# Optimization experiments

Hardware: AMD Instinct MI355X
Metric: run time of the kernel (lower is better)

## Reference

```python
import jax, jax.numpy as jnp
import numpy as np

N_FEATURES = 170
D_MODEL = 64
N_HEADS = 4
ALPHA = 0.1
LN_EPS = 1e-5
LEAKY_SLOPE = 0.01  # torch F.leaky_relu default
N = 3 * N_FEATURES  # 510
B = 32


def setup_inputs() -> dict:
    key = jax.random.key(0)
    ks = jax.random.split(key, 10)
    D, H = D_MODEL, N_HEADS
    s = 1.0 / np.sqrt(D)
    return {
        "x": jax.random.normal(ks[0], (B, N, D), dtype=jnp.float32),
        "causal_graph": jax.random.uniform(ks[1], (N, N), dtype=jnp.float32),
        # nn.Linear(d_model, d_model*n_heads, bias=False): stored here as (D, H*D) for x @ W
        "W": jax.random.uniform(ks[2], (D, H * D), jnp.float32, -s, s),
        "attention_w": jax.random.normal(ks[3], (H, 2 * D), dtype=jnp.float32),
        # Conv2d(2, n_heads, 3, padding=1): OIHW kernel
        "conv_w": jax.random.uniform(ks[4], (H, 2, 3, 3), jnp.float32, -1/np.sqrt(18), 1/np.sqrt(18)),
        "conv_b": jax.random.uniform(ks[5], (H,), jnp.float32, -1/np.sqrt(18), 1/np.sqrt(18)),
        # nn.Linear(d_model, 2*d_model): stored as (D, 2D)
        "fcg_w": jax.random.uniform(ks[6], (D, 2 * D), jnp.float32, -s, s),
        "fcg_b": jax.random.uniform(ks[7], (2 * D,), jnp.float32, -s, s),
        "ln_g": jnp.ones((D,), jnp.float32),
        "ln_b": jnp.zeros((D,), jnp.float32),
    }


def reference(x, causal_graph, W, attention_w, conv_w, conv_b, fcg_w, fcg_b, ln_g, ln_b):
    Bz, Nn, D = x.shape
    H = N_HEADS
    # shared projection: (B, N, H, D)
    xt = (x @ W).reshape(Bz, Nn, H, D)
    # GAT-style additive scores: concat-dot decomposed into two dot products
    w1, w2 = attention_w[:, :D], attention_w[:, D:]  # each (H, D)
    s_i = jnp.einsum('bnhd,hd->bhn', xt, w1)  # source term
    s_j = jnp.einsum('bnhd,hd->bhn', xt, w2)  # target term
    e = s_i[:, :, :, None] + s_j[:, :, None, :]  # (B, H, N, N)
    A_eva = jnp.where(e >= 0, e, LEAKY_SLOPE * e)  # leaky_relu
    # fuse mean attention with causal graph via 3x3 conv
    A_mean = A_eva.mean(axis=1)  # (B, N, N)
    causal = jnp.broadcast_to(causal_graph[None], (Bz, Nn, Nn))
    stacked = jnp.stack([A_mean, causal], axis=1)  # (B, 2, N, N)
    A_st = jax.lax.conv_general_dilated(
        stacked, conv_w, window_strides=(1, 1), padding=((1, 1), (1, 1)),
        dimension_numbers=('NCHW', 'OIHW', 'NCHW'))
    A_st = A_st + conv_b[None, :, None, None]  # (B, H, N, N)
    A = jax.nn.softmax(ALPHA * A_eva + (1.0 - ALPHA) * A_st, axis=-1)
    # multi-head aggregation then head-mean
    out = jnp.einsum('bhnm,bmhd->bnhd', A, xt).mean(axis=2)  # (B, N, D)
    # GLU
    g = out @ fcg_w + fcg_b  # (B, N, 2D)
    a, b = g[..., :D], g[..., D:]
    glu = a * jax.nn.sigmoid(b)
    # residual + layernorm
    y = glu + x
    mu = y.mean(axis=-1, keepdims=True)
    var = ((y - mu) ** 2).mean(axis=-1, keepdims=True)
    y = (y - mu) * jax.lax.rsqrt(var + LN_EPS) * ln_g + ln_b
    return y, A
```

## Files before the change

### kernel.cpp

```cpp
#include <hip/hip_runtime.h>

#define Bz 32
#define Nn 510
#define Dd 64
#define Hh 4
#define HD_ 256
#define Kpad 512
#define ALPHA_ 0.1f
#define LNEPS 1e-5f
#define SLOPE 0.01f
#define NEG_INF -3.0e38f

typedef __attribute__((ext_vector_type(8))) short short8;
typedef __attribute__((ext_vector_type(4))) float floatx4;

__device__ inline float wredsum(float v) {
  #pragma unroll
  for (int off = 32; off; off >>= 1) v += __shfl_xor(v, off, 64);
  return v;
}
__device__ inline float wredmax(float v) {
  #pragma unroll
  for (int off = 32; off; off >>= 1) v = fmaxf(v, __shfl_xor(v, off, 64));
  return v;
}
__device__ inline unsigned short f2bf(float f) {
  unsigned int u = __float_as_uint(f);
  unsigned int r = (u + 0x7fffu + ((u >> 16) & 1u)) >> 16;
  return (unsigned short)r;
}

__global__ __launch_bounds__(256) void k1_xt(const float* __restrict__ x,
                                             const float* __restrict__ W,
                                             const float* __restrict__ attw,
                                             unsigned short* __restrict__ xtT,
                                             float* __restrict__ si,
                                             float* __restrict__ sj) {
  __shared__ float Wl[64][132];
  __shared__ float xr[32][68];
  const int t = threadIdx.x;
  const int rt = blockIdx.x;
  const int b = blockIdx.y;
  const int ch = blockIdx.z;
  #pragma unroll
  for (int k = 0; k < 8; k++) {
    int f = t + k * 256;
    int kr = f >> 5;
    int c = (f & 31) * 4;
    float4 v = *(const float4*)&W[kr * HD_ + ch * 128 + c];
    *(float4*)&Wl[kr][c] = v;
  }
  #pragma unroll
  for (int k = 0; k < 2; k++) {
    int f = t + k * 256;
    int r = f >> 4;
    int c = (f & 15) * 4;
    int row = rt * 32 + r;
    float4 v = make_float4(0.f, 0.f, 0.f, 0.f);
    if (row < Nn) v = *(const float4*)&x[(b * Nn + row) * Dd + c];
    *(float4*)&xr[r][c] = v;
  }
  __syncthreads();
  const int tr = t >> 5, tc = t & 31;
  const int rb = tr * 4, c0 = tc * 4;
  float acc[4][4] = {};
  #pragma unroll
  for (int k4 = 0; k4 < 16; k4++) {
    float4 xv[4];
    #pragma unroll
    for (int r = 0; r < 4; r++) xv[r] = *(float4*)&xr[rb + r][k4 * 4];
    #pragma unroll
    for (int kk = 0; kk < 4; kk++) {
      float4 wv = *(float4*)&Wl[k4 * 4 + kk][c0];
      #pragma unroll
      for (int r = 0; r < 4; r++) {
        float xs = (&xv[r].x)[kk];
        acc[r][0] = fmaf(xs, wv.x, acc[r][0]);
        acc[r][1] = fmaf(xs, wv.y, acc[r][1]);
        acc[r][2] = fmaf(xs, wv.z, acc[r][2]);
        acc[r][3] = fmaf(xs, wv.w, acc[r][3]);
      }
    }
  }
  const int colbase = ch * 128 + c0;
  const int h = colbase >> 6;
  const int dd = colbase & 63;
  const int m0r = rt * 32 + rb;
  #pragma unroll
  for (int cc = 0; cc < 4; cc++) {
    unsigned short* p = &xtT[((size_t)(b * 4 + h) * 64 + (dd + cc)) * Kpad + m0r];
    if (m0r + 3 < Nn) {
      ushort4 u;
      u.x = f2bf(acc[0][cc]); u.y = f2bf(acc[1][cc]);
      u.z = f2bf(acc[2][cc]); u.w = f2bf(acc[3][cc]);
      *(ushort4*)p = u;
    } else {
      #pragma unroll
      for (int r = 0; r < 4; r++) if (m0r + r < Nn) p[r] = f2bf(acc[r][cc]);
    }
  }
  float w1v[4], w2v[4];
  #pragma unroll
  for (int cc = 0; cc < 4; cc++) {
    w1v[cc] = attw[h * 128 + dd + cc];
    w2v[cc] = attw[h * 128 + 64 + dd + cc];
  }
  #pragma unroll
  for (int r = 0; r < 4; r++) {
    float p1 = acc[r][0] * w1v[0] + acc[r][1] * w1v[1] +
               acc[r][2] * w1v[2] + acc[r][3] * w1v[3];
    float p2 = acc[r][0] * w2v[0] + acc[r][1] * w2v[1] +
               acc[r][2] * w2v[2] + acc[r][3] * w2v[3];
    #pragma unroll
    for (int off = 1; off <= 8; off <<= 1) {
      p1 += __shfl_xor(p1, off, 64);
      p2 += __shfl_xor(p2, off, 64);
    }
    if ((tc & 15) == 0) {
      int row = m0r + r;
      if (row < Nn) {
        si[(b * 4 + h) * Nn + row] = p1;
        sj[(b * 4 + h) * Nn + row] = p2;
      }
    }
  }
}

__global__ __launch_bounds__(256) void k2_attn(const float* __restrict__ si,
                                               const float* __restrict__ sj,
                                               const float* __restrict__ causal,
                                               const float* __restrict__ convw,
                                               const float* __restrict__ convb,
                                               float* __restrict__ A) {
  __shared__ float amr[3][520];
  __shared__ float c3[3][520];
  const int t = threadIdx.x;
  const int i = blockIdx.x;
  const int b = blockIdx.y;
  for (int e = t; e < 3 * 520; e += 256) {
    int row = e / 520;
    int jj = e - row * 520;
    int iq = i + row - 1;
    int j = jj - 1;
    float am = 0.f, cz = 0.f;
    if (jj < 512 && iq >= 0 && iq < Nn && j >= 0 && j < Nn) {
      float s = 0.f;
      #pragma unroll
      for (int hh = 0; hh < 4; hh++) {
        float e2 = si[(b * 4 + hh) * Nn + iq] + sj[(b * 4 + hh) * Nn + j];
        s += (e2 >= 0.f) ? e2 : SLOPE * e2;
      }
      am = 0.25f * s;
      cz = causal[iq * Nn + j];
    }
    amr[row][jj] = am;
    c3[row][jj] = cz;
  }
  __syncthreads();
  const int h = t >> 6;
  const int lane = t & 63;
  const int j0 = lane * 8;
  const int bh = b * 4 + h;
  const float sih = si[bh * Nn + i];
  float cw[18];
  #pragma unroll
  for (int q = 0; q < 18; q++) cw[q] = convw[h * 18 + q];
  float conv[8];
  const float cb = convb[h];
  #pragma unroll
  for (int e = 0; e < 8; e++) conv[e] = cb;
  #pragma unroll
  for (int di = 0; di < 3; di++) {
    float ta[12], tcc[12];
    *(float4*)&ta[0] = *(float4*)&amr[di][j0];
    *(float4*)&ta[4] = *(float4*)&amr[di][j0 + 4];
    *(float4*)&ta[8] = *(float4*)&amr[di][j0 + 8];
    *(float4*)&tcc[0] = *(float4*)&c3[di][j0];
    *(float4*)&tcc[4] = *(float4*)&c3[di][j0 + 4];
    *(float4*)&tcc[8] = *(float4*)&c3[di][j0 + 8];
    float w0 = cw[di * 3], w1 = cw[di * 3 + 1], w2 = cw[di * 3 + 2];
    float u0 = cw[9 + di * 3], u1 = cw[9 + di * 3 + 1], u2 = cw[9 + di * 3 + 2];
    #pragma unroll
    for (int e = 0; e < 8; e++) {
      float cv = conv[e];
      cv = fmaf(w0, ta[e], cv);
      cv = fmaf(w1, ta[e + 1], cv);
      cv = fmaf(w2, ta[e + 2], cv);
      cv = fmaf(u0, tcc[e], cv);
      cv = fmaf(u1, tcc[e + 1], cv);
      cv = fmaf(u2, tcc[e + 2], cv);
      conv[e] = cv;
    }
  }
  float sjv[8];
  {
    const float* sp = &sj[bh * Nn + j0];
    *(float2*)&sjv[0] = *(const float2*)&sp[0];
    *(float2*)&sjv[2] = *(const float2*)&sp[2];
    *(float2*)&sjv[4] = *(const float2*)&sp[4];
    *(float2*)&sjv[6] = *(const float2*)&sp[6];
  }
  float v[8];
  float mx = NEG_INF;
  #pragma unroll
  for (int e = 0; e < 8; e++) {
    float ee = sih + sjv[e];
    float l = (ee >= 0.f) ? ee : SLOPE * ee;
    float val = ALPHA_ * l + (1.0f - ALPHA_) * conv[e];
    v[e] = (j0 + e < Nn) ? val : NEG_INF;
    mx = fmaxf(mx, v[e]);
  }
  mx = wredmax(mx);
  float p[8], s = 0.f;
  #pragma unroll
  for (int e = 0; e < 8; e++) {
    p[e] = __expf(v[e] - mx);
    s += p[e];
  }
  s = wredsum(s);
  const float inv = 1.f / s;
  float* Ar = &A[((size_t)bh * Nn + i) * Nn];
  #pragma unroll
  for (int pr = 0; pr < 4; pr++) {
    if (j0 + 2 * pr + 1 < Nn) {
      float2 w2v = make_float2(p[2 * pr] * inv, p[2 * pr + 1] * inv);
      *(float2*)&Ar[j0 + 2 * pr] = w2v;
    }
  }
}

__global__ __launch_bounds__(256) void k3_out(const float* __restrict__ A,
                                              const unsigned short* __restrict__ xtT,
                                              const float* __restrict__ x,
                                              const float* __restrict__ fcgw,
                                              const float* __restrict__ fcgb,
                                              const float* __restrict__ lng,
                                              const float* __restrict__ lnb,
                                              float* __restrict__ y) {
  __shared__ unsigned short Asub[32 * 72];
  __shared__ unsigned short Xsub[64 * 72];
  __shared__ float ol[32][64];
  __shared__ float gl[2][128];
  const int t = threadIdx.x;
  const int n0 = blockIdx.x * 32;
  const int b = blockIdx.y;
  const int w = t >> 6, lane = t & 63;
  const int quad = lane >> 4, l16 = lane & 15;
  const int wr = (w & 1) * 16;
  const int wc = (w >> 1) * 32;
  const int ar = t >> 3;
  const int amc = (t & 7) * 8;
  const int xd = t >> 2;
  const int xmc = (t & 3) * 16;
  floatx4 acc0 = {0.f, 0.f, 0.f, 0.f};
  floatx4 acc1 = {0.f, 0.f, 0.f, 0.f};
  for (int h = 0; h < 4; h++) {
    const float* Ab = &A[((size_t)(b * 4 + h) * Nn + n0) * Nn];
    const unsigned short* Xb = &xtT[(size_t)(b * 4 + h) * 64 * Kpad];
    for (int kt = 0; kt < 8; kt++) {
      const int m0 = kt * 64;
      __syncthreads();
      {
        int n = n0 + ar;
        int m = m0 + amc;
        float av[8] = {0.f, 0.f, 0.f, 0.f, 0.f, 0.f, 0.f, 0.f};
        if (n < Nn) {
          const float* src = &Ab[(size_t)ar * Nn + m];
          if (m + 7 < Nn) {
            #pragma unroll
            for (int q = 0; q < 4; q++) *(float2*)&av[2 * q] = *(const float2*)&src[2 * q];
          } else {
            int lim = Nn - m;
            #pragma unroll
            for (int q = 0; q < 8; q++) if (q < lim) av[q] = src[q];
          }
        }
        short8 as;
        #pragma unroll
        for (int q = 0; q < 8; q++) as[q] = (short)f2bf(av[q]);
        *(short8*)&Asub[ar * 72 + amc] = as;
        const unsigned short* xs = &Xb[(size_t)xd * Kpad + m0 + xmc];
        short8 x0 = *(const short8*)&xs[0];
        short8 x1 = *(const short8*)&xs[8];
        *(short8*)&Xsub[xd * 72 + xmc] = x0;
        *(short8*)&Xsub[xd * 72 + xmc + 8] = x1;
      }
      __syncthreads();
      #pragma unroll
      for (int ks = 0; ks < 2; ks++) {
        short8 af = *(short8*)&Asub[(wr + l16) * 72 + ks * 32 + quad * 8];
        short8 b0 = *(short8*)&Xsub[(wc + l16) * 72 + ks * 32 + quad * 8];
        short8 b1 = *(short8*)&Xsub[(wc + 16 + l16) * 72 + ks * 32 + quad * 8];
        acc0 = __builtin_amdgcn_mfma_f32_16x16x32_bf16(af, b0, acc0, 0, 0, 0);
        acc1 = __builtin_amdgcn_mfma_f32_16x16x32_bf16(af, b1, acc1, 0, 0, 0);
      }
    }
  }
  __syncthreads();
  #pragma unroll
  for (int reg = 0; reg < 4; reg++) {
    ol[wr + quad * 4 + reg][wc + l16] = 0.25f * acc0[reg];
    ol[wr + quad * 4 + reg][wc + 16 + l16] = 0.25f * acc1[reg];
  }
  __syncthreads();
  const int kk = t & 127;
  const int rg = t >> 7;
  for (int it = 0; it < 16; it++) {
    const int r = it * 2 + rg;
    const int row = n0 + r;
    float g = fcgb[kk];
    #pragma unroll
    for (int d = 0; d < 64; d++) g = fmaf(ol[r][d], fcgw[d * 128 + kk], g);
    gl[rg][kk] = g;
    __syncthreads();
    if (kk < 64 && row < Nn) {
      float a = gl[rg][kk];
      float bb = gl[rg][kk + 64];
      float glu = a / (1.f + __expf(-bb));
      float yv = glu + x[(b * Nn + row) * Dd + kk];
      float mu = wredsum(yv) * (1.f / 64.f);
      float dv = yv - mu;
      float var = wredsum(dv * dv) * (1.f / 64.f);
      float o = dv * rsqrtf(var + LNEPS) * lng[kk] + lnb[kk];
      y[(b * Nn + row) * Dd + kk] = o;
    }
    __syncthreads();
  }
}

extern "C" void kernel_launch(void* const* d_in, const int* in_sizes, int n_in,
                              void* d_out, int out_size, void* d_ws, size_t ws_size,
                              hipStream_t stream) {
  const float* x      = (const float*)d_in[0];
  const float* causal = (const float*)d_in[1];
  const float* W      = (const float*)d_in[2];
  const float* attw   = (const float*)d_in[3];
  const float* convw  = (const float*)d_in[4];
  const float* convb  = (const float*)d_in[5];
  const float* fcgw   = (const float*)d_in[6];
  const float* fcgb   = (const float*)d_in[7];
  const float* lng    = (const float*)d_in[8];
  const float* lnb    = (const float*)d_in[9];

  float* ws = (float*)d_ws;
  float* si = ws;
  float* sj = si + (size_t)Bz * Hh * Nn;
  unsigned short* xtT = (unsigned short*)(sj + (size_t)Bz * Hh * Nn + 16);
  size_t xtT_bytes = (size_t)Bz * Hh * Dd * Kpad * sizeof(unsigned short);

  float* yout = (float*)d_out;
  float* Aout = yout + (size_t)Bz * Nn * Dd;

  hipMemsetAsync(xtT, 0, xtT_bytes, stream);
  k1_xt <<<dim3(16, Bz, 2), 256, 0, stream>>>(x, W, attw, xtT, si, sj);
  k2_attn<<<dim3(Nn, Bz), 256, 0, stream>>>(si, sj, causal, convw, convb, Aout);
  k3_out<<<dim3(16, Bz), 256, 0, stream>>>(Aout, xtT, x, fcgw, fcgb, lng, lnb, yout);
}
```

Before: 309.9 us.

## Tile attention kernel over 8 rows with transposed LDS layout; halve output tile

The attention kernel now handles 8 query rows per block instead of 1. It stages si/sj and a 10-row halo of mean-attention and causal values in LDS using a transposed, padded layout, so each causal/score row is loaded once and reused by up to three output rows instead of being recomputed per row. The A stores become float4 writes. The aggregation kernel moves to 16-row tiles, giving twice as many blocks for better occupancy, at the cost of re-reading the xt tiles more often.

```diff
diff --git a/kernel.cpp b/kernel.cpp
--- a/kernel.cpp
+++ b/kernel.cpp
@@ -132,99 +132,121 @@
                                                const float* __restrict__ convw,
                                                const float* __restrict__ convb,
                                                float* __restrict__ A) {
-  __shared__ float amr[3][520];
-  __shared__ float c3[3][520];
+  __shared__ float am_t[10 * 8 * 68];
+  __shared__ float cz_t[10 * 8 * 68];
+  __shared__ float sjl[4 * 8 * 68];
+  __shared__ float sil[4][12];
   const int t = threadIdx.x;
-  const int i = blockIdx.x;
+  const int i0 = blockIdx.x * 8;
   const int b = blockIdx.y;
-  for (int e = t; e < 3 * 520; e += 256) {
-    int row = e / 520;
-    int jj = e - row * 520;
-    int iq = i + row - 1;
-    int j = jj - 1;
+  if (t < 40) {
+    int h = t / 10, r = t % 10;
+    int iq = i0 + r - 1;
+    sil[h][r] = (iq >= 0 && iq < Nn) ? si[(b * 4 + h) * Nn + iq] : 0.f;
+  }
+  if (t >= 64 && t < 224) {
+    int q = t - 64;
+    int r = q >> 4, rem = q & 15;
+    int e = rem >> 1, side = rem & 1;
+    int idx = (r * 8 + e) * 68 + side * 65;
+    am_t[idx] = 0.f;
+    cz_t[idx] = 0.f;
+  }
+  for (int f = t; f < 2048; f += 256) {
+    int h = f >> 9, j = f & 511;
+    float v = (j < Nn) ? sj[(b * 4 + h) * Nn + j] : 0.f;
+    sjl[(h * 8 + (j & 7)) * 68 + (j >> 3) + 1] = v;
+  }
+  __syncthreads();
+  for (int f = t; f < 5120; f += 256) {
+    int r = f >> 9, j = f & 511;
+    int iq = i0 + r - 1;
     float am = 0.f, cz = 0.f;
-    if (jj < 512 && iq >= 0 && iq < Nn && j >= 0 && j < Nn) {
+    if (iq >= 0 && iq < Nn && j < Nn) {
       float s = 0.f;
       #pragma unroll
-      for (int hh = 0; hh < 4; hh++) {
-        float e2 = si[(b * 4 + hh) * Nn + iq] + sj[(b * 4 + hh) * Nn + j];
+      for (int h = 0; h < 4; h++) {
+        float e2 = sil[h][r] + sjl[(h * 8 + (j & 7)) * 68 + (j >> 3) + 1];
         s += (e2 >= 0.f) ? e2 : SLOPE * e2;
       }
       am = 0.25f * s;
       cz = causal[iq * Nn + j];
     }
-    amr[row][jj] = am;
-    c3[row][jj] = cz;
-  }
-  __syncthreads();
-  const int h = t >> 6;
-  const int lane = t & 63;
-  const int j0 = lane * 8;
-  const int bh = b * 4 + h;
-  const float sih = si[bh * Nn + i];
-  float cw[18];
-  #pragma unroll
-  for (int q = 0; q < 18; q++) cw[q] = convw[h * 18 + q];
-  float conv[8];
-  const float cb = convb[h];
-  #pragma unroll
-  for (int e = 0; e < 8; e++) conv[e] = cb;
-  #pragma unroll
-  for (int di = 0; di < 3; di++) {
-    float ta[12], tcc[12];
-    *(float4*)&ta[0] = *(float4*)&amr[di][j0];
-    *(float4*)&ta[4] = *(float4*)&amr[di][j0 + 4];
-    *(float4*)&ta[8] = *(float4*)&amr[di][j0 + 8];
-    *(float4*)&tcc[0] = *(float4*)&c3[di][j0];
-    *(float4*)&tcc[4] = *(float4*)&c3[di][j0 + 4];
-    *(float4*)&tcc[8] = *(float4*)&c3[di][j0 + 8];
-    float w0 = cw[di * 3], w1 = cw[di * 3 + 1], w2 = cw[di * 3 + 2];
-    float u0 = cw[9 + di * 3], u1 = cw[9 + di * 3 + 1], u2 = cw[9 + di * 3 + 2];
+    int idx = (r * 8 + (j & 7)) * 68 + (j >> 3) + 1;
+    am_t[idx] = am;
+    cz_t[idx] = cz;
+  }
+  __syncthreads();
+  const int w = t >> 6, L = t & 63;
+  const int j0 = L * 8;
+  for (int pp = w; pp < 32; pp += 4) {
+    const int il = pp >> 2, h = pp & 3;
+    const int i = i0 + il;
+    if (i >= Nn) continue;
+    const int bh = b * 4 + h;
+    const float sih = sil[h][il + 1];
+    float cw[18];
+    #pragma unroll
+    for (int q = 0; q < 18; q++) cw[q] = convw[h * 18 + q];
+    const float cb = convb[h];
+    float conv[8];
+    #pragma unroll
+    for (int e = 0; e < 8; e++) conv[e] = cb;
+    #pragma unroll
+    for (int r3 = 0; r3 < 3; r3++) {
+      const float* ba = &am_t[((il + r3) * 8) * 68];
+      const float* bc = &cz_t[((il + r3) * 8) * 68];
+      float a[10], c[10];
+      a[0] = ba[7 * 68 + L];
+      c[0] = bc[7 * 68 + L];
+      #pragma unroll
+      for (int e = 0; e < 8; e++) {
+        a[1 + e] = ba[e * 68 + L + 1];
+        c[1 + e] = bc[e * 68 + L + 1];
+      }
+      a[9] = ba[0 * 68 + L + 2];
+      c[9] = bc[0 * 68 + L + 2];
+      float w0 = cw[r3 * 3], w1 = cw[r3 * 3 + 1], w2 = cw[r3 * 3 + 2];
+      float u0 = cw[9 + r3 * 3], u1 = cw[9 + r3 * 3 + 1], u2 = cw[9 + r3 * 3 + 2];
+      #pragma unroll
+      for (int e = 0; e < 8; e++) {
+        float cv = conv[e];
+        cv = fmaf(w0, a[e], cv);
+        cv = fmaf(w1, a[e + 1], cv);
+        cv = fmaf(w2, a[e + 2], cv);
+        cv = fmaf(u0, c[e], cv);
+        cv = fmaf(u1, c[e + 1], cv);
+        cv = fmaf(u2, c[e + 2], cv);
+        conv[e] = cv;
+      }
+    }
+    float v[8];
+    float mx = NEG_INF;
     #pragma unroll
     for (int e = 0; e < 8; e++) {
-      float cv = conv[e];
-      cv = fmaf(w0, ta[e], cv);
-      cv = fmaf(w1, ta[e + 1], cv);
-      cv = fmaf(w2, ta[e + 2], cv);
-      cv = fmaf(u0, tcc[e], cv);
-      cv = fmaf(u1, tcc[e + 1], cv);
-      cv = fmaf(u2, tcc[e + 2], cv);
-      conv[e] = cv;
-    }
-  }
-  float sjv[8];
-  {
-    const float* sp = &sj[bh * Nn + j0];
-    *(float2*)&sjv[0] = *(const float2*)&sp[0];
-    *(float2*)&sjv[2] = *(const float2*)&sp[2];
-    *(float2*)&sjv[4] = *(const float2*)&sp[4];
-    *(float2*)&sjv[6] = *(const float2*)&sp[6];
-  }
-  float v[8];
-  float mx = NEG_INF;
-  #pragma unroll
-  for (int e = 0; e < 8; e++) {
-    float ee = sih + sjv[e];
-    float l = (ee >= 0.f) ? ee : SLOPE * ee;
-    float val = ALPHA_ * l + (1.0f - ALPHA_) * conv[e];
-    v[e] = (j0 + e < Nn) ? val : NEG_INF;
-    mx = fmaxf(mx, v[e]);
-  }
-  mx = wredmax(mx);
-  float p[8], s = 0.f;
-  #pragma unroll
-  for (int e = 0; e < 8; e++) {
-    p[e] = __expf(v[e] - mx);
-    s += p[e];
-  }
-  s = wredsum(s);
-  const float inv = 1.f / s;
-  float* Ar = &A[((size_t)bh * Nn + i) * Nn];
-  #pragma unroll
-  for (int pr = 0; pr < 4; pr++) {
-    if (j0 + 2 * pr + 1 < Nn) {
-      float2 w2v = make_float2(p[2 * pr] * inv, p[2 * pr + 1] * inv);
-      *(float2*)&Ar[j0 + 2 * pr] = w2v;
+      float ee = sih + sjl[(h * 8 + e) * 68 + L + 1];
+      float l = (ee >= 0.f) ? ee : SLOPE * ee;
+      float val = ALPHA_ * l + (1.0f - ALPHA_) * conv[e];
+      v[e] = (j0 + e < Nn) ? val : NEG_INF;
+      mx = fmaxf(mx, v[e]);
+    }
+    mx = wredmax(mx);
+    float p[8], s = 0.f;
+    #pragma unroll
+    for (int e = 0; e < 8; e++) {
+      p[e] = __expf(v[e] - mx);
+      s += p[e];
+    }
+    s = wredsum(s);
+    const float inv = 1.f / s;
+    #pragma unroll
+    for (int e = 0; e < 8; e++) p[e] *= inv;
+    float* Ar = &A[((size_t)bh * Nn + i) * Nn + j0];
+    *(float4*)&Ar[0] = make_float4(p[0], p[1], p[2], p[3]);
+    if (L < 63) {
+      *(float4*)&Ar[4] = make_float4(p[4], p[5], p[6], p[7]);
+    } else {
+      *(float2*)&Ar[4] = make_float2(p[4], p[5]);
     }
   }
 }
@@ -237,23 +259,21 @@
                                               const float* __restrict__ lng,
                                               const float* __restrict__ lnb,
                                               float* __restrict__ y) {
-  __shared__ unsigned short Asub[32 * 72];
+  __shared__ unsigned short Asub[16 * 72];
   __shared__ unsigned short Xsub[64 * 72];
-  __shared__ float ol[32][64];
+  __shared__ float ol[16][64];
   __shared__ float gl[2][128];
   const int t = threadIdx.x;
-  const int n0 = blockIdx.x * 32;
+  const int n0 = blockIdx.x * 16;
   const int b = blockIdx.y;
   const int w = t >> 6, lane = t & 63;
   const int quad = lane >> 4, l16 = lane & 15;
-  const int wr = (w & 1) * 16;
-  const int wc = (w >> 1) * 32;
-  const int ar = t >> 3;
-  const int amc = (t & 7) * 8;
+  const int wc = w * 16;
+  const int ar = t >> 4;
+  const int amc = (t & 15) * 4;
   const int xd = t >> 2;
   const int xmc = (t & 3) * 16;
-  floatx4 acc0 = {0.f, 0.f, 0.f, 0.f};
-  floatx4 acc1 = {0.f, 0.f, 0.f, 0.f};
+  floatx4 acc = {0.f, 0.f, 0.f, 0.f};
   for (int h = 0; h < 4; h++) {
     const float* Ab = &A[((size_t)(b * 4 + h) * Nn + n0) * Nn];
     const unsigned short* Xb = &xtT[(size_t)(b * 4 + h) * 64 * Kpad];
@@ -263,22 +283,21 @@
       {
         int n = n0 + ar;
         int m = m0 + amc;
-        float av[8] = {0.f, 0.f, 0.f, 0.f, 0.f, 0.f, 0.f, 0.f};
+        float av[4] = {0.f, 0.f, 0.f, 0.f};
         if (n < Nn) {
           const float* src = &Ab[(size_t)ar * Nn + m];
-          if (m + 7 < Nn) {
-            #pragma unroll
-            for (int q = 0; q < 4; q++) *(float2*)&av[2 * q] = *(const float2*)&src[2 * q];
+          if (m + 3 < Nn) {
+            *(float4*)av = *(const float4*)src;
           } else {
             int lim = Nn - m;
             #pragma unroll
-            for (int q = 0; q < 8; q++) if (q < lim) av[q] = src[q];
+            for (int q = 0; q < 4; q++) if (q < lim) av[q] = src[q];
           }
         }
-        short8 as;
-        #pragma unroll
-        for (int q = 0; q < 8; q++) as[q] = (short)f2bf(av[q]);
-        *(short8*)&Asub[ar * 72 + amc] = as;
+        ushort4 u;
+        u.x = f2bf(av[0]); u.y = f2bf(av[1]);
+        u.z = f2bf(av[2]); u.w = f2bf(av[3]);
+        *(ushort4*)&Asub[ar * 72 + amc] = u;
         const unsigned short* xs = &Xb[(size_t)xd * Kpad + m0 + xmc];
         short8 x0 = *(const short8*)&xs[0];
         short8 x1 = *(const short8*)&xs[8];
@@ -288,24 +307,21 @@
       __syncthreads();
       #pragma unroll
       for (int ks = 0; ks < 2; ks++) {
-        short8 af = *(short8*)&Asub[(wr + l16) * 72 + ks * 32 + quad * 8];
-        short8 b0 = *(short8*)&Xsub[(wc + l16) * 72 + ks * 32 + quad * 8];
-        short8 b1 = *(short8*)&Xsub[(wc + 16 + l16) * 72 + ks * 32 + quad * 8];
-        acc0 = __builtin_amdgcn_mfma_f32_16x16x32_bf16(af, b0, acc0, 0, 0, 0);
-        acc1 = __builtin_amdgcn_mfma_f32_16x16x32_bf16(af, b1, acc1, 0, 0, 0);
+        short8 af = *(short8*)&Asub[l16 * 72 + ks * 32 + quad * 8];
+        short8 bf = *(short8*)&Xsub[(wc + l16) * 72 + ks * 32 + quad * 8];
+        acc = __builtin_amdgcn_mfma_f32_16x16x32_bf16(af, bf, acc, 0, 0, 0);
       }
     }
   }
   __syncthreads();
   #pragma unroll
   for (int reg = 0; reg < 4; reg++) {
-    ol[wr + quad * 4 + reg][wc + l16] = 0.25f * acc0[reg];
-    ol[wr + quad * 4 + reg][wc + 16 + l16] = 0.25f * acc1[reg];
+    ol[quad * 4 + reg][wc + l16] = 0.25f * acc[reg];
   }
   __syncthreads();
   const int kk = t & 127;
   const int rg = t >> 7;
-  for (int it = 0; it < 16; it++) {
+  for (int it = 0; it < 8; it++) {
     const int r = it * 2 + rg;
     const int row = n0 + r;
     float g = fcgb[kk];
@@ -353,6 +369,6 @@
 
   hipMemsetAsync(xtT, 0, xtT_bytes, stream);
   k1_xt <<<dim3(16, Bz, 2), 256, 0, stream>>>(x, W, attw, xtT, si, sj);
-  k2_attn<<<dim3(Nn, Bz), 256, 0, stream>>>(si, sj, causal, convw, convb, Aout);
-  k3_out<<<dim3(16, Bz), 256, 0, stream>>>(Aout, xtT, x, fcgw, fcgb, lng, lnb, yout);
-}
+  k2_attn<<<dim3(64, Bz), 256, 0, stream>>>(si, sj, causal, convw, convb, Aout);
+  k3_out <<<dim3(32, Bz), 256, 0, stream>>>(Aout, xtT, x, fcgw, fcgb, lng, lnb, yout);
+}
```

Result: no change. 308.5 us (-0.5%).
